# Kernel optimization log

Measured on AMD Instinct MI355X. Metric: run time of the kernel, lower is better.

The kernel has to match this reference:

```python
import jax, jax.numpy as jnp
import numpy as np
import math

N_HEADS = 32
N_GROUPS = 8
D_HEAD = 64  # d_queries = d_values
D_MODEL = 2048


def _rope(x):
    # lucidrains-style interleaved RoPE over the full head dim, offset=0.
    # x: (B, H, S, D)
    S, D = x.shape[-2], x.shape[-1]
    inv_freq = 1.0 / (10000.0 ** (jnp.arange(0, D, 2, dtype=jnp.float32) / D))  # (D/2,)
    freqs = jnp.arange(S, dtype=jnp.float32)[:, None] * inv_freq[None, :]       # (S, D/2)
    cos = jnp.repeat(jnp.cos(freqs), 2, axis=-1)  # (S, D) interleaved
    sin = jnp.repeat(jnp.sin(freqs), 2, axis=-1)
    x2 = x.reshape(*x.shape[:-1], D // 2, 2)
    rot = jnp.stack([-x2[..., 1], x2[..., 0]], axis=-1).reshape(x.shape)
    return x * cos + rot * sin


def setup_inputs() -> dict:
    key = jax.random.key(0)
    ks = jax.random.split(key, 6)
    hidden_states = jax.random.normal(ks[0], (2, 2048, D_MODEL), dtype=jnp.float32)
    s = 0.02
    Wq = jax.random.normal(ks[1], (D_MODEL, N_HEADS * D_HEAD), dtype=jnp.float32) * s
    Wk = jax.random.normal(ks[2], (D_MODEL, N_GROUPS * D_HEAD), dtype=jnp.float32) * s
    Wv = jax.random.normal(ks[3], (D_MODEL, N_GROUPS * D_HEAD), dtype=jnp.float32) * s
    Wo = jax.random.normal(ks[4], (N_HEADS * D_HEAD, D_MODEL), dtype=jnp.float32) * s
    bo = jnp.zeros((D_MODEL,), dtype=jnp.float32)
    return {"hidden_states": hidden_states, "Wq": Wq, "Wk": Wk, "Wv": Wv, "Wo": Wo, "bo": bo}


def reference(hidden_states, Wq, Wk, Wv, Wo, bo):
    N, S, _ = hidden_states.shape
    n_rep = N_HEADS // N_GROUPS
    q = (hidden_states @ Wq).reshape(N, S, N_HEADS, D_HEAD).transpose(0, 2, 1, 3)
    k = (hidden_states @ Wk).reshape(N, S, N_GROUPS, D_HEAD).transpose(0, 2, 1, 3)
    v = (hidden_states @ Wv).reshape(N, S, N_GROUPS, D_HEAD).transpose(0, 2, 1, 3)
    q = _rope(q)
    k = _rope(k)
    # GQA: repeat_interleave KV heads
    k = jnp.repeat(k, n_rep, axis=1)
    v = jnp.repeat(v, n_rep, axis=1)
    scores = jnp.einsum('bhsd,bhtd->bhst', q, k)  # (B, H, S, S)
    # ALiBi bias added BEFORE scaling (matches source order)
    slopes = 2.0 ** (-(jnp.arange(1, N_HEADS + 1, dtype=jnp.float32) * 8.0 / N_HEADS))
    pos = jnp.arange(S, dtype=jnp.float32)
    alibi = -jnp.abs(pos[:, None] - pos[None, :])[None] * slopes[:, None, None]  # (H, S, S)
    scores = (scores + alibi[None]) / math.sqrt(D_HEAD)
    # grok-style rescaling
    scores = 30.0 * jnp.tanh(scores / 30.0)
    causal = jnp.tril(jnp.ones((S, S), dtype=bool))
    scores = jnp.where(causal[None, None], scores, -jnp.inf)
    probs = jax.nn.softmax(scores, axis=-1)
    ctx = jnp.einsum('bhst,bhtd->bhsd', probs, v)
    ctx = ctx.transpose(0, 2, 1, 3).reshape(N, S, N_HEADS * D_HEAD)
    return ctx @ Wo + bo
```

## Files before the change

### kernel.cpp

```cpp
#include <hip/hip_runtime.h>
#include <hip/hip_bf16.h>
#include <math.h>

#define DMODEL 2048
#define SEQ    2048
#define NH     32
#define NG     8
#define DH     64

typedef unsigned short u16;
using v8bf  = __attribute__((ext_vector_type(8))) __bf16;
using f32x4 = __attribute__((ext_vector_type(4))) float;

__device__ __forceinline__ float bf2f(u16 u) {
    unsigned int x = ((unsigned int)u) << 16;
    return __uint_as_float(x);
}
__device__ __forceinline__ u16 f2bf(float f) {
    unsigned int x = __float_as_uint(f);
    unsigned int r = (x + 0x7fffu + ((x >> 16) & 1u)) >> 16;
    return (u16)r;
}
__device__ __forceinline__ u16 f2bf_hw(float f) {
    __bf16 b = (__bf16)f;
    return __builtin_bit_cast(u16, b);
}
__device__ __forceinline__ f32x4 mfma16(v8bf a, v8bf b, f32x4 c) {
    return __builtin_amdgcn_mfma_f32_16x16x32_bf16(a, b, c, 0, 0, 0);
}

#define LOG1E4_64 0.14391156509880297f
#define LOG2E     1.4426950408889634f

#define C_HS   0u
#define C_WQ   8388608u
#define C_WK   12582912u
#define C_WV   13631488u
#define C_WO   14680064u
#define C_BO   18874368u
#define W_Q    18876416u
#define W_K    27265024u
#define W_V    29362176u
#define W_CTX  31459328u

__device__ __forceinline__ bool detect_is_f32(const u16* hsu, int tid, float* red, int nw)
{
    ushort4 a = *(const ushort4*)(hsu + tid * 8);
    ushort4 b = *(const ushort4*)(hsu + tid * 8 + 4);
    u16 vals[8] = {a.x, a.y, a.z, a.w, b.x, b.y, b.z, b.w};
    float mymax = 0.0f;
    #pragma unroll
    for (int e = 0; e < 8; ++e) {
        float av = fabsf(bf2f(vals[e]));
        if (!(av < 1.0e30f)) av = 1.0e30f;
        mymax = fmaxf(mymax, av);
    }
    #pragma unroll
    for (int off = 1; off < 64; off <<= 1)
        mymax = fmaxf(mymax, __shfl_xor(mymax, off, 64));
    if ((tid & 63) == 0) red[tid >> 6] = mymax;
    __syncthreads();
    float m = red[0];
    for (int i = 1; i < nw; ++i) m = fmaxf(m, red[i]);
    __syncthreads();
    return m > 1.0e6f;
}

__global__ __launch_bounds__(256)
void conv_hs_bo(const void* __restrict__ hs, const void* __restrict__ bo,
                u16* __restrict__ canon)
{
    __shared__ float red[4];
    const int tid = threadIdx.x;
    const bool is_f32 = detect_is_f32((const u16*)hs, tid, red, 4);
    unsigned int g = (blockIdx.x * 256u + tid) * 8u;
    const void* src; unsigned int loc; u16* dst;
    if (g < 8388608u) { src = hs; loc = g;            dst = canon + C_HS + g; }
    else              { src = bo; loc = g - 8388608u; dst = canon + C_BO + loc; }

    ushort4 o0, o1;
    if (is_f32) {
        const float* f = (const float*)src + loc;
        float4 x = *(const float4*)f;
        float4 y = *(const float4*)(f + 4);
        o0.x = f2bf(x.x); o0.y = f2bf(x.y); o0.z = f2bf(x.z); o0.w = f2bf(x.w);
        o1.x = f2bf(y.x); o1.y = f2bf(y.y); o1.z = f2bf(y.z); o1.w = f2bf(y.w);
    } else {
        const u16* u = (const u16*)src + loc;
        o0 = *(const ushort4*)u;
        o1 = *(const ushort4*)(u + 4);
    }
    *(ushort4*)dst       = o0;
    *(ushort4*)(dst + 4) = o1;
}

__global__ __launch_bounds__(256)
void transp_w(const void* __restrict__ W, u16* __restrict__ dst,
              int K, int N, const u16* __restrict__ hs_orig)
{
    __shared__ float red[4];
    __shared__ u16 Ts[64][68];
    const int tid = threadIdx.x;
    const bool is_f32 = detect_is_f32(hs_orig, tid, red, 4);
    const int n0 = blockIdx.x * 64, k0 = blockIdx.y * 64;

    #pragma unroll
    for (int it = 0; it < 4; ++it) {
        int e  = tid + it * 256;
        int kr = e >> 4, n4 = (e & 15) << 2;
        if (is_f32) {
            const float* s = (const float*)W + (size_t)(k0 + kr) * N + n0 + n4;
            float4 x = *(const float4*)s;
            Ts[n4+0][kr] = f2bf(x.x); Ts[n4+1][kr] = f2bf(x.y);
            Ts[n4+2][kr] = f2bf(x.z); Ts[n4+3][kr] = f2bf(x.w);
        } else {
            ushort4 u = *(const ushort4*)((const u16*)W + (size_t)(k0 + kr) * N + n0 + n4);
            Ts[n4+0][kr] = u.x; Ts[n4+1][kr] = u.y;
            Ts[n4+2][kr] = u.z; Ts[n4+3][kr] = u.w;
        }
    }
    __syncthreads();
    #pragma unroll
    for (int it = 0; it < 4; ++it) {
        int e  = tid + it * 256;
        int nr = e >> 4, k4 = (e & 15) << 2;
        ushort4 u;
        u.x = Ts[nr][k4+0]; u.y = Ts[nr][k4+1];
        u.z = Ts[nr][k4+2]; u.w = Ts[nr][k4+3];
        *(ushort4*)(dst + (size_t)(n0 + nr) * K + k0 + k4) = u;
    }
}

__global__ __launch_bounds__(256)
void rope_table(float* __restrict__ c, float* __restrict__ s)
{
    int idx = blockIdx.x * 256 + threadIdx.x;
    int sq = idx >> 6, d = idx & 63;
    float freq = expf(-(float)(d & ~1) * LOG1E4_64);
    float sn, cs;
    sincosf((float)sq * freq, &sn, &cs);
    c[idx] = cs; s[idx] = sn;
}

__global__ __launch_bounds__(512, 4) __attribute__((amdgpu_waves_per_eu(4, 4)))
void gemm_qkv(const u16* __restrict__ hs, const u16* __restrict__ wqt,
              const u16* __restrict__ wkt, const u16* __restrict__ wvt,
              const float* __restrict__ ropec, const float* __restrict__ ropes,
              u16* __restrict__ qws, u16* __restrict__ kws, u16* __restrict__ vws)
{
    __shared__ __align__(16) u16 As[128][72];
    __shared__ __align__(16) u16 Bs[128][72];
    const int tid = threadIdx.x;
    const int w = tid >> 6, lane = tid & 63;
    const int l15 = lane & 15, quad = lane >> 4;
    const int wr = (w >> 2) * 64, wc = (w & 3) * 32;
    const int row0 = blockIdx.x * 128;
    const int n0   = blockIdx.y * 128;

    const u16* Wt; int nb, mode;
    if (n0 < 2048)      { Wt = wqt; nb = n0;        mode = 0; }
    else if (n0 < 2560) { Wt = wkt; nb = n0 - 2048; mode = 1; }
    else                { Wt = wvt; nb = n0 - 2560; mode = 2; }

    const int r0 = tid >> 3, c0 = (tid & 7) * 8;
    const u16* arow = hs + (size_t)(row0 + r0) * DMODEL + c0;
    const u16* brow = Wt + (size_t)(nb   + r0) * DMODEL + c0;

    f32x4 acc[4][2];
    #pragma unroll
    for (int mt = 0; mt < 4; ++mt)
        #pragma unroll
        for (int nt = 0; nt < 2; ++nt)
            acc[mt][nt] = (f32x4){0.f, 0.f, 0.f, 0.f};

    for (int k0 = 0; k0 < DMODEL; k0 += 64) {
        __syncthreads();
        *(uint4*)&As[r0][c0]      = *(const uint4*)(arow + k0);
        *(uint4*)&As[r0 + 64][c0] = *(const uint4*)(arow + (size_t)64 * DMODEL + k0);
        *(uint4*)&Bs[r0][c0]      = *(const uint4*)(brow + k0);
        *(uint4*)&Bs[r0 + 64][c0] = *(const uint4*)(brow + (size_t)64 * DMODEL + k0);
        __syncthreads();
        #pragma unroll
        for (int ks = 0; ks < 2; ++ks) {
            v8bf a[4], b[2];
            #pragma unroll
            for (int mt = 0; mt < 4; ++mt)
                a[mt] = *(const v8bf*)&As[wr + 16*mt + l15][ks*32 + quad*8];
            #pragma unroll
            for (int nt = 0; nt < 2; ++nt)
                b[nt] = *(const v8bf*)&Bs[wc + 16*nt + l15][ks*32 + quad*8];
            #pragma unroll
            for (int mt = 0; mt < 4; ++mt)
                #pragma unroll
                for (int nt = 0; nt < 2; ++nt)
                    acc[mt][nt] = mfma16(a[mt], b[nt], acc[mt][nt]);
        }
    }

    #pragma unroll
    for (int mt = 0; mt < 4; ++mt) {
        #pragma unroll
        for (int nt = 0; nt < 2; ++nt) {
            int col  = n0 + wc + 16*nt + l15;
            int dcol = col & 63;
            #pragma unroll
            for (int reg = 0; reg < 4; ++reg) {
                int row = row0 + wr + 16*mt + quad*4 + reg;
                int b = row >> 11, s = row & (SEQ - 1);
                float val = acc[mt][nt][reg];
                if (mode < 2) {
                    float c2 = ropec[(s << 6) + dcol];
                    float s2 = ropes[(s << 6) + dcol];
                    float partner = __shfl_xor(val, 1, 64);
                    val = (dcol & 1) ? (val * c2 + partner * s2)
                                     : (val * c2 - partner * s2);
                }
                if (mode == 0) {
                    int h = col >> 6;
                    qws[((size_t)((b*NH + h) * SEQ + s)) * DH + dcol] = f2bf_hw(val);
                } else if (mode == 1) {
                    int g = (col - 2048) >> 6;
                    kws[((size_t)((b*NG + g) * SEQ + s)) * DH + dcol] = f2bf_hw(val);
                } else {
                    int g = (col - 2560) >> 6;
                    vws[((size_t)((b*NG + g) * DH + dcol)) * SEQ + s] = f2bf_hw(val);
                }
            }
        }
    }
}

__global__ __launch_bounds__(256, 4)
void attn(const u16* __restrict__ qws, const u16* __restrict__ kws,
          const u16* __restrict__ vws, u16* __restrict__ ctx)
{
    __shared__ __align__(16) u16 Ks[64][72];
    __shared__ __align__(16) u16 Vs[64][72];
    __shared__ __align__(16) u16 Ps[4][16][72];
    const int tid = threadIdx.x;
    const int w = tid >> 6, lane = tid & 63;
    const int l15 = lane & 15, quad = lane >> 4;
    const int sr = tid >> 3;
    const int sc = (tid & 7) * 8;

    const int h = blockIdx.y, b = blockIdx.z;
    const int g = h >> 2;

    const float slope = exp2f(-0.25f * (float)(h + 1));
    const u16* kbase  = kws + (size_t)(b*NG + g) * SEQ * DH;
    const u16* vtbase = vws + (size_t)(b*NG + g) * DH * SEQ;
    const u16* qhead  = qws + (size_t)(b*NH + h) * SEQ * DH;

    const float Ac = 0.125f * (LOG2E / 15.0f);
    const float Bc = -slope * 0.125f * (LOG2E / 15.0f);
    const float C3 = -60.0f * LOG2E;
    float bd[4][4];
    #pragma unroll
    for (int nt = 0; nt < 4; ++nt)
        #pragma unroll
        for (int reg = 0; reg < 4; ++reg)
            bd[nt][reg] = Bc * (float)((16*w + 4*quad + reg) - (16*nt + l15));

    uint4 rk0, rk1, rv0, rv1;

#define LOADG(kt_) do {                                                       \
    const u16* kp_ = kbase + (size_t)(kt_) * (64 * DH);                       \
    rk0 = *(const uint4*)(kp_ + sr * DH + sc);                                \
    rk1 = *(const uint4*)(kp_ + (sr + 32) * DH + sc);                         \
    const u16* vp_ = vtbase + (size_t)(kt_) * 64;                             \
    rv0 = *(const uint4*)(vp_ + (size_t)sr * SEQ + sc);                       \
    rv1 = *(const uint4*)(vp_ + (size_t)(sr + 32) * SEQ + sc);                \
} while (0)

#define STORELDS() do {                                                       \
    *(uint4*)&Ks[sr][sc]      = rk0;                                          \
    *(uint4*)&Ks[sr + 32][sc] = rk1;                                          \
    *(uint4*)&Vs[sr][sc]      = rv0;                                          \
    *(uint4*)&Vs[sr + 32][sc] = rv1;                                          \
} while (0)

#define COMPUTE(kt_, DIAGC) do {                                              \
    f32x4 sacc_[4];                                                           \
    _Pragma("unroll")                                                         \
    for (int nt_ = 0; nt_ < 4; ++nt_) sacc_[nt_] = (f32x4){0.f,0.f,0.f,0.f};  \
    _Pragma("unroll")                                                         \
    for (int ks_ = 0; ks_ < 2; ++ks_)                                         \
        _Pragma("unroll")                                                     \
        for (int nt_ = 0; nt_ < 4; ++nt_) {                                   \
            v8bf kf_ = *(const v8bf*)&Ks[16*nt_ + l15][ks_*32 + quad*8];      \
            sacc_[nt_] = mfma16(qa[ks_], kf_, sacc_[nt_]);                    \
        }                                                                     \
    const float tb_ = Bc * (float)(q0 - (kt_) * 64);                          \
    _Pragma("unroll")                                                         \
    for (int nt_ = 0; nt_ < 4; ++nt_) {                                       \
        _Pragma("unroll")                                                     \
        for (int rg_ = 0; rg_ < 4; ++rg_) {                                   \
            float arg_ = fmaf(sacc_[nt_][rg_], Ac, bd[nt_][rg_] + tb_);       \
            float wv_  = __builtin_amdgcn_exp2f(arg_);                        \
            float rr_  = __builtin_amdgcn_rcpf(wv_ + 1.0f);                   \
            float pv_  = __builtin_amdgcn_exp2f(rr_ * C3);                    \
            if (DIAGC && (16*nt_ + l15) > (16*w + 4*quad + rg_)) pv_ = 0.0f;  \
            lrow[rg_] += pv_;                                                 \
            Ps[w][quad*4 + rg_][16*nt_ + l15] = f2bf_hw(pv_);                 \
        }                                                                     \
    }                                                                         \
    _Pragma("unroll")                                                         \
    for (int ks_ = 0; ks_ < 2; ++ks_) {                                       \
        v8bf pa_ = *(const v8bf*)&Ps[w][l15][ks_*32 + quad*8];                \
        _Pragma("unroll")                                                     \
        for (int dt_ = 0; dt_ < 4; ++dt_) {                                   \
            v8bf vf_ = *(const v8bf*)&Vs[16*dt_ + l15][ks_*32 + quad*8];      \
            o[dt_] = mfma16(pa_, vf_, o[dt_]);                                \
        }                                                                     \
    }                                                                         \
} while (0)

    #pragma unroll 1
    for (int half = 0; half < 2; ++half) {
        const int qt = half ? 31 - (int)blockIdx.x : (int)blockIdx.x;
        const int q0 = qt * 64;

        const u16* qrow = qhead + (size_t)(q0 + 16*w + l15) * DH;
        v8bf qa[2];
        qa[0] = *(const v8bf*)(qrow + 0*32 + quad*8);
        qa[1] = *(const v8bf*)(qrow + 1*32 + quad*8);

        f32x4 o[4];
        #pragma unroll
        for (int dt = 0; dt < 4; ++dt) o[dt] = (f32x4){0.f, 0.f, 0.f, 0.f};
        float lrow[4] = {0.f, 0.f, 0.f, 0.f};

        LOADG(0);
        for (int kt = 0; kt < qt; ++kt) {
            STORELDS();
            __syncthreads();
            LOADG(kt + 1);
            COMPUTE(kt, 0);
            __syncthreads();
        }
        STORELDS();
        __syncthreads();
        COMPUTE(qt, 1);
        __syncthreads();

        #pragma unroll
        for (int reg = 0; reg < 4; ++reg) {
            float lr = lrow[reg];
            #pragma unroll
            for (int off = 1; off < 16; off <<= 1)
                lr += __shfl_xor(lr, off, 64);
            float linv = __builtin_amdgcn_rcpf(lr);
            int s = q0 + 16*w + quad*4 + reg;
            u16* crow = ctx + (size_t)(b*SEQ + s) * DMODEL + h*64 + l15;
            #pragma unroll
            for (int dt = 0; dt < 4; ++dt)
                crow[16*dt] = f2bf_hw(o[dt][reg] * linv);
        }
    }
#undef LOADG
#undef STORELDS
#undef COMPUTE
}

__global__ __launch_bounds__(512, 4) __attribute__((amdgpu_waves_per_eu(4, 4)))
void oproj(const u16* __restrict__ ctx, const u16* __restrict__ wot,
           const u16* __restrict__ bo, const u16* __restrict__ hs_orig,
           void* __restrict__ outp)
{
    __shared__ float red[8];
    __shared__ __align__(16) u16 As[128][72];
    __shared__ __align__(16) u16 Bs[128][72];
    const int tid = threadIdx.x;
    const bool is_f32 = detect_is_f32(hs_orig, tid, red, 8);
    const int w = tid >> 6, lane = tid & 63;
    const int l15 = lane & 15, quad = lane >> 4;
    const int wr = (w >> 2) * 64, wc = (w & 3) * 32;
    const int row0 = blockIdx.x * 128;
    const int n0   = blockIdx.y * 128;

    const int r0 = tid >> 3, c0 = (tid & 7) * 8;
    const u16* arow = ctx + (size_t)(row0 + r0) * DMODEL + c0;
    const u16* brow = wot + (size_t)(n0   + r0) * DMODEL + c0;

    f32x4 acc[4][2];
    #pragma unroll
    for (int mt = 0; mt < 4; ++mt)
        #pragma unroll
        for (int nt = 0; nt < 2; ++nt)
            acc[mt][nt] = (f32x4){0.f, 0.f, 0.f, 0.f};

    for (int k0 = 0; k0 < DMODEL; k0 += 64) {
        __syncthreads();
        *(uint4*)&As[r0][c0]      = *(const uint4*)(arow + k0);
        *(uint4*)&As[r0 + 64][c0] = *(const uint4*)(arow + (size_t)64 * DMODEL + k0);
        *(uint4*)&Bs[r0][c0]      = *(const uint4*)(brow + k0);
        *(uint4*)&Bs[r0 + 64][c0] = *(const uint4*)(brow + (size_t)64 * DMODEL + k0);
        __syncthreads();
        #pragma unroll
        for (int ks = 0; ks < 2; ++ks) {
            v8bf a[4], b[2];
            #pragma unroll
            for (int mt = 0; mt < 4; ++mt)
                a[mt] = *(const v8bf*)&As[wr + 16*mt + l15][ks*32 + quad*8];
            #pragma unroll
            for (int nt = 0; nt < 2; ++nt)
                b[nt] = *(const v8bf*)&Bs[wc + 16*nt + l15][ks*32 + quad*8];
            #pragma unroll
            for (int mt = 0; mt < 4; ++mt)
                #pragma unroll
                for (int nt = 0; nt < 2; ++nt)
                    acc[mt][nt] = mfma16(a[mt], b[nt], acc[mt][nt]);
        }
    }

    #pragma unroll
    for (int mt = 0; mt < 4; ++mt) {
        #pragma unroll
        for (int nt = 0; nt < 2; ++nt) {
            int col = n0 + wc + 16*nt + l15;
            float bias = bf2f(bo[col]);
            #pragma unroll
            for (int reg = 0; reg < 4; ++reg) {
                int row = row0 + wr + 16*mt + quad*4 + reg;
                float val = acc[mt][nt][reg] + bias;
                if (is_f32) ((float*)outp)[(size_t)row * DMODEL + col] = val;
                else        ((u16*)outp)[(size_t)row * DMODEL + col]   = f2bf(val);
            }
        }
    }
}

extern "C" void kernel_launch(void* const* d_in, const int* in_sizes, int n_in,
                              void* d_out, int out_size, void* d_ws, size_t ws_size,
                              hipStream_t stream) {
    u16* ws = (u16*)d_ws;
    u16* canon = ws;
    u16* qws = ws + W_Q;
    u16* kws = ws + W_K;
    u16* vws = ws + W_V;
    u16* ctxp = ws + W_CTX;
    float* ropec = (float*)(ws + W_CTX);
    float* ropes = ropec + SEQ * DH;
    const u16* hs_raw = (const u16*)d_in[0];

    conv_hs_bo<<<dim3(4097), 256, 0, stream>>>(d_in[0], d_in[5], canon);
    transp_w<<<dim3(32, 32), 256, 0, stream>>>(d_in[1], canon + C_WQ, 2048, 2048, hs_raw);
    transp_w<<<dim3(8, 32),  256, 0, stream>>>(d_in[2], canon + C_WK, 2048, 512, hs_raw);
    transp_w<<<dim3(8, 32),  256, 0, stream>>>(d_in[3], canon + C_WV, 2048, 512, hs_raw);
    transp_w<<<dim3(32, 32), 256, 0, stream>>>(d_in[4], canon + C_WO, 2048, 2048, hs_raw);
    rope_table<<<dim3(512), 256, 0, stream>>>(ropec, ropes);
    gemm_qkv<<<dim3(32, 24), 512, 0, stream>>>(canon + C_HS, canon + C_WQ,
        canon + C_WK, canon + C_WV, ropec, ropes, qws, kws, vws);
    attn<<<dim3(16, NH, 2), 256, 0, stream>>>(qws, kws, vws, ctxp);
    oproj<<<dim3(32, 16), 512, 0, stream>>>(ctxp, canon + C_WO, canon + C_BO, hs_raw, d_out);
}
```

Before: 348.3 us.

## Prefetch GEMM tiles into registers and transpose attention score MFMA layout

The QKV and output projection GEMMs now load the next K-tile from global memory into registers while the current tile is being multiplied, a register-staged software pipeline that hides global load latency. The attention kernel swaps the MFMA operands so each lane holds scores for one query row across four keys. This lets the probability tile be written to LDS as packed 64-bit stores instead of scalar 16-bit stores, and collapses the row-sum reduction to two shuffles. The cost is extra registers for the prefetch buffers, which could hurt occupancy under the fixed launch bounds.

```diff
diff --git a/kernel.cpp b/kernel.cpp
--- a/kernel.cpp
+++ b/kernel.cpp
@@ -9,6 +9,7 @@
 #define DH     64
 
 typedef unsigned short u16;
+typedef unsigned int u32;
 using v8bf  = __attribute__((ext_vector_type(8))) __bf16;
 using f32x4 = __attribute__((ext_vector_type(4))) float;
 
@@ -24,6 +25,9 @@
 __device__ __forceinline__ u16 f2bf_hw(float f) {
     __bf16 b = (__bf16)f;
     return __builtin_bit_cast(u16, b);
+}
+__device__ __forceinline__ u32 f2bf_pk(float lo, float hi) {
+    return (u32)f2bf_hw(lo) | ((u32)f2bf_hw(hi) << 16);
 }
 __device__ __forceinline__ f32x4 mfma16(v8bf a, v8bf b, f32x4 c) {
     return __builtin_amdgcn_mfma_f32_16x16x32_bf16(a, b, c, 0, 0, 0);
@@ -173,13 +177,25 @@
         for (int nt = 0; nt < 2; ++nt)
             acc[mt][nt] = (f32x4){0.f, 0.f, 0.f, 0.f};
 
+    uint4 ra0, ra1, rb0, rb1;
+#define LOADG(k0_) do {                                                       \
+    ra0 = *(const uint4*)(arow + (k0_));                                      \
+    ra1 = *(const uint4*)(arow + (size_t)64 * DMODEL + (k0_));                \
+    rb0 = *(const uint4*)(brow + (k0_));                                      \
+    rb1 = *(const uint4*)(brow + (size_t)64 * DMODEL + (k0_));                \
+} while (0)
+#define STORELDS() do {                                                       \
+    *(uint4*)&As[r0][c0]      = ra0;                                          \
+    *(uint4*)&As[r0 + 64][c0] = ra1;                                          \
+    *(uint4*)&Bs[r0][c0]      = rb0;                                          \
+    *(uint4*)&Bs[r0 + 64][c0] = rb1;                                          \
+} while (0)
+
+    LOADG(0);
     for (int k0 = 0; k0 < DMODEL; k0 += 64) {
-        __syncthreads();
-        *(uint4*)&As[r0][c0]      = *(const uint4*)(arow + k0);
-        *(uint4*)&As[r0 + 64][c0] = *(const uint4*)(arow + (size_t)64 * DMODEL + k0);
-        *(uint4*)&Bs[r0][c0]      = *(const uint4*)(brow + k0);
-        *(uint4*)&Bs[r0 + 64][c0] = *(const uint4*)(brow + (size_t)64 * DMODEL + k0);
-        __syncthreads();
+        STORELDS();
+        __syncthreads();
+        if (k0 + 64 < DMODEL) LOADG(k0 + 64);
         #pragma unroll
         for (int ks = 0; ks < 2; ++ks) {
             v8bf a[4], b[2];
@@ -195,7 +211,10 @@
                 for (int nt = 0; nt < 2; ++nt)
                     acc[mt][nt] = mfma16(a[mt], b[nt], acc[mt][nt]);
         }
-    }
+        __syncthreads();
+    }
+#undef LOADG
+#undef STORELDS
 
     #pragma unroll
     for (int mt = 0; mt < 4; ++mt) {
@@ -254,12 +273,12 @@
     const float Ac = 0.125f * (LOG2E / 15.0f);
     const float Bc = -slope * 0.125f * (LOG2E / 15.0f);
     const float C3 = -60.0f * LOG2E;
-    float bd[4][4];
-    #pragma unroll
-    for (int nt = 0; nt < 4; ++nt)
+    float bdw[4][4];
+    #pragma unroll
+    for (int mt = 0; mt < 4; ++mt)
         #pragma unroll
         for (int reg = 0; reg < 4; ++reg)
-            bd[nt][reg] = Bc * (float)((16*w + 4*quad + reg) - (16*nt + l15));
+            bdw[mt][reg] = Bc * (float)((16*w + l15) - (16*mt + 4*quad + reg));
 
     uint4 rk0, rk1, rv0, rv1;
 
@@ -282,27 +301,32 @@
 #define COMPUTE(kt_, DIAGC) do {                                              \
     f32x4 sacc_[4];                                                           \
     _Pragma("unroll")                                                         \
-    for (int nt_ = 0; nt_ < 4; ++nt_) sacc_[nt_] = (f32x4){0.f,0.f,0.f,0.f};  \
+    for (int mt_ = 0; mt_ < 4; ++mt_) sacc_[mt_] = (f32x4){0.f,0.f,0.f,0.f};  \
     _Pragma("unroll")                                                         \
     for (int ks_ = 0; ks_ < 2; ++ks_)                                         \
         _Pragma("unroll")                                                     \
-        for (int nt_ = 0; nt_ < 4; ++nt_) {                                   \
-            v8bf kf_ = *(const v8bf*)&Ks[16*nt_ + l15][ks_*32 + quad*8];      \
-            sacc_[nt_] = mfma16(qa[ks_], kf_, sacc_[nt_]);                    \
+        for (int mt_ = 0; mt_ < 4; ++mt_) {                                   \
+            v8bf kf_ = *(const v8bf*)&Ks[16*mt_ + l15][ks_*32 + quad*8];      \
+            sacc_[mt_] = mfma16(kf_, qa[ks_], sacc_[mt_]);                    \
         }                                                                     \
     const float tb_ = Bc * (float)(q0 - (kt_) * 64);                          \
     _Pragma("unroll")                                                         \
-    for (int nt_ = 0; nt_ < 4; ++nt_) {                                       \
+    for (int mt_ = 0; mt_ < 4; ++mt_) {                                       \
+        float pv_[4];                                                         \
         _Pragma("unroll")                                                     \
         for (int rg_ = 0; rg_ < 4; ++rg_) {                                   \
-            float arg_ = fmaf(sacc_[nt_][rg_], Ac, bd[nt_][rg_] + tb_);       \
+            float arg_ = fmaf(sacc_[mt_][rg_], Ac, bdw[mt_][rg_] + tb_);      \
             float wv_  = __builtin_amdgcn_exp2f(arg_);                        \
             float rr_  = __builtin_amdgcn_rcpf(wv_ + 1.0f);                   \
-            float pv_  = __builtin_amdgcn_exp2f(rr_ * C3);                    \
-            if (DIAGC && (16*nt_ + l15) > (16*w + 4*quad + rg_)) pv_ = 0.0f;  \
-            lrow[rg_] += pv_;                                                 \
-            Ps[w][quad*4 + rg_][16*nt_ + l15] = f2bf_hw(pv_);                 \
+            float p_   = __builtin_amdgcn_exp2f(rr_ * C3);                    \
+            if (DIAGC && (16*mt_ + 4*quad + rg_) > (16*w + l15)) p_ = 0.0f;   \
+            lsum += p_;                                                       \
+            pv_[rg_] = p_;                                                    \
         }                                                                     \
+        uint2 pk_;                                                            \
+        pk_.x = f2bf_pk(pv_[0], pv_[1]);                                      \
+        pk_.y = f2bf_pk(pv_[2], pv_[3]);                                      \
+        *(uint2*)&Ps[w][l15][16*mt_ + quad*4] = pk_;                          \
     }                                                                         \
     _Pragma("unroll")                                                         \
     for (int ks_ = 0; ks_ < 2; ++ks_) {                                       \
@@ -328,7 +352,7 @@
         f32x4 o[4];
         #pragma unroll
         for (int dt = 0; dt < 4; ++dt) o[dt] = (f32x4){0.f, 0.f, 0.f, 0.f};
-        float lrow[4] = {0.f, 0.f, 0.f, 0.f};
+        float lsum = 0.0f;
 
         LOADG(0);
         for (int kt = 0; kt < qt; ++kt) {
@@ -343,13 +367,12 @@
         COMPUTE(qt, 1);
         __syncthreads();
 
+        float lr = lsum;
+        lr += __shfl_xor(lr, 16, 64);
+        lr += __shfl_xor(lr, 32, 64);
         #pragma unroll
         for (int reg = 0; reg < 4; ++reg) {
-            float lr = lrow[reg];
-            #pragma unroll
-            for (int off = 1; off < 16; off <<= 1)
-                lr += __shfl_xor(lr, off, 64);
-            float linv = __builtin_amdgcn_rcpf(lr);
+            float linv = __builtin_amdgcn_rcpf(__shfl(lr, quad*4 + reg, 64));
             int s = q0 + 16*w + quad*4 + reg;
             u16* crow = ctx + (size_t)(b*SEQ + s) * DMODEL + h*64 + l15;
             #pragma unroll
@@ -389,13 +412,25 @@
         for (int nt = 0; nt < 2; ++nt)
             acc[mt][nt] = (f32x4){0.f, 0.f, 0.f, 0.f};
 
+    uint4 ra0, ra1, rb0, rb1;
+#define LOADG(k0_) do {                                                       \
+    ra0 = *(const uint4*)(arow + (k0_));                                      \
+    ra1 = *(const uint4*)(arow + (size_t)64 * DMODEL + (k0_));                \
+    rb0 = *(const uint4*)(brow + (k0_));                                      \
+    rb1 = *(const uint4*)(brow + (size_t)64 * DMODEL + (k0_));                \
+} while (0)
+#define STORELDS() do {                                                       \
+    *(uint4*)&As[r0][c0]      = ra0;                                          \
+    *(uint4*)&As[r0 + 64][c0] = ra1;                                          \
+    *(uint4*)&Bs[r0][c0]      = rb0;                                          \
+    *(uint4*)&Bs[r0 + 64][c0] = rb1;                                          \
+} while (0)
+
+    LOADG(0);
     for (int k0 = 0; k0 < DMODEL; k0 += 64) {
-        __syncthreads();
-        *(uint4*)&As[r0][c0]      = *(const uint4*)(arow + k0);
-        *(uint4*)&As[r0 + 64][c0] = *(const uint4*)(arow + (size_t)64 * DMODEL + k0);
-        *(uint4*)&Bs[r0][c0]      = *(const uint4*)(brow + k0);
-        *(uint4*)&Bs[r0 + 64][c0] = *(const uint4*)(brow + (size_t)64 * DMODEL + k0);
-        __syncthreads();
+        STORELDS();
+        __syncthreads();
+        if (k0 + 64 < DMODEL) LOADG(k0 + 64);
         #pragma unroll
         for (int ks = 0; ks < 2; ++ks) {
             v8bf a[4], b[2];
@@ -411,7 +446,10 @@
                 for (int nt = 0; nt < 2; ++nt)
                     acc[mt][nt] = mfma16(a[mt], b[nt], acc[mt][nt]);
         }
-    }
+        __syncthreads();
+    }
+#undef LOADG
+#undef STORELDS
 
     #pragma unroll
     for (int mt = 0; mt < 4; ++mt) {
```

Result: faster. 339.9 us (-2.4%).
